# Kernel optimization log

Measured on AMD Instinct MI355X. Metric: run time of the kernel, lower is better.

## Reference

```python
import jax, jax.numpy as jnp
import numpy as np

C = 768      # token feature dim
N = 196      # tokens per stream
R_DIM = 2 * 2 * N  # 784 = concat(A row, A col)


def setup_inputs() -> dict:
    key = jax.random.key(0)
    ks = jax.random.split(key, 16)
    s = 1.0 / np.sqrt(C)
    inp = {
        "x": jax.random.normal(ks[0], (128, N, C), dtype=jnp.float32),
        "y": jax.random.normal(ks[1], (128, N, C), dtype=jnp.float32),
        # linear_conv_1: 1x1 conv (768->768) + BN affine (eval) + ReLU
        "W1": jax.random.normal(ks[2], (C, C), dtype=jnp.float32) * s,
        "b1": jnp.zeros((C,), dtype=jnp.float32),
        "g1": jax.random.uniform(ks[3], (C,), dtype=jnp.float32, minval=0.5, maxval=1.5),
        "be1": jax.random.normal(ks[4], (C,), dtype=jnp.float32) * 0.1,
        # linear_conv_2
        "W2": jax.random.normal(ks[5], (C, C), dtype=jnp.float32) * s,
        "b2": jnp.zeros((C,), dtype=jnp.float32),
        "g2": jax.random.uniform(ks[6], (C,), dtype=jnp.float32, minval=0.5, maxval=1.5),
        "be2": jax.random.normal(ks[7], (C,), dtype=jnp.float32) * 0.1,
        # linear_conv_3: 768->768
        "W3": jax.random.normal(ks[8], (C, C), dtype=jnp.float32) * s,
        "b3": jnp.zeros((C,), dtype=jnp.float32),
        # linear_conv_4: 784->784 over relation rows
        "W4": jax.random.normal(ks[9], (784, 784), dtype=jnp.float32) / np.sqrt(784.0),
        "b4": jnp.zeros((784,), dtype=jnp.float32),
        # linear_conv_5: (768+784)->1
        "W5": jax.random.normal(ks[10], (C + 784, 1), dtype=jnp.float32) / np.sqrt(C + 784.0),
        "b5": jnp.zeros((1,), dtype=jnp.float32),
    }
    return inp


def reference(x, y, W1, b1, g1, be1, W2, b2, g2, be2, W3, b3, W4, b4, W5, b5):
    # per-token 1x1 conv + BN(eval)->affine + ReLU
    phi_x = jax.nn.relu((x @ W1 + b1) * g1 + be1)          # [B,196,768]
    phi_y = jax.nn.relu((y @ W2 + b2) * g2 + be2)          # [B,196,768]
    cat_phi = jnp.concatenate([phi_x, phi_y], axis=1)      # [B,392,768]
    # affinity matrix A = cat_phi @ cat_phi^T
    A = jnp.einsum("bnd,bmd->bnm", cat_phi, cat_phi)       # [B,392,392]
    # R[i] = concat(A[i,:], A[:,i]) -> vectorized as [A | A^T]
    R = jnp.concatenate([A, jnp.swapaxes(A, 1, 2)], axis=2)  # [B,392,784]
    v = cat_phi @ W3 + b3                                   # [B,392,768]
    v_ = R @ W4 + b4                                        # [B,392,784]
    cat_v = jnp.concatenate([v, v_], axis=2)                # [B,392,1552]
    W = cat_v @ W5 + b5                                     # [B,392,1]
    # per-token reweighting then sum of the two streams
    out = x * W[:, :N, :] + y * W[:, N:, :]                 # [B,196,768]
    return out
```

## Files before the change

### kernel.cpp

```cpp
#include <hip/hip_runtime.h>

typedef __bf16 bf16_t;
typedef bf16_t bf16x8 __attribute__((ext_vector_type(8)));
typedef float f32x4 __attribute__((ext_vector_type(4)));
typedef float f32x16 __attribute__((ext_vector_type(16)));
typedef unsigned short u16x8 __attribute__((ext_vector_type(8)));
typedef unsigned short u16x4 __attribute__((ext_vector_type(4)));

#define CD 768
#define NT 196
#define NB 128
#define T2 392
#define MROWS (NB*NT)
#define NTILE 1176

__device__ __forceinline__ unsigned short f2bf(float f){
  unsigned u = __float_as_uint(f);
  u += 0x7fffu + ((u >> 16) & 1u);
  return (unsigned short)(u >> 16);
}
__device__ __forceinline__ float bf2f(unsigned short h){
  return __uint_as_float(((unsigned)h) << 16);
}
__device__ __forceinline__ float wave_reduce(float v){
  #pragma unroll
  for (int o = 32; o > 0; o >>= 1) v += __shfl_down(v, o, 64);
  return v;
}
__device__ __forceinline__ void gload16(const unsigned short* g, unsigned short* l){
  __builtin_amdgcn_global_load_lds(
      (const __attribute__((address_space(1))) unsigned int*)g,
      (__attribute__((address_space(3))) unsigned int*)l, 16, 0, 0);
}

__global__ __launch_bounds__(256) void prep_pack(const float* __restrict__ W1,
                        const float* __restrict__ W2,
                        unsigned short* __restrict__ W1p, unsigned short* __restrict__ W2p){
  __shared__ float tile[64][33];
  const float* src = blockIdx.z ? W2 : W1;
  unsigned short* dst = blockIdx.z ? W2p : W1p;
  const int kt = blockIdx.x, g = blockIdx.y, tid = threadIdx.x;
  #pragma unroll
  for (int e = 0; e < 8; ++e){
    int idx = e*256 + tid;
    int kk = idx >> 5, nn = idx & 31;
    tile[kk][nn] = src[(size_t)(kt*64 + kk)*CD + g*32 + nn];
  }
  __syncthreads();
  const int ks = tid >> 6, lane = tid & 63;
  const int l31 = lane & 31, lh = lane >> 5;
  unsigned short* o = dst + ((size_t)((g*12 + kt)*4 + ks)*64 + lane)*8;
  #pragma unroll
  for (int i = 0; i < 8; ++i)
    o[i] = f2bf(tile[ks*16 + lh*8 + i][l31]);
}

__global__ void prep_u(const float* __restrict__ W3, const float* __restrict__ W4,
                       const float* __restrict__ W5, const float* __restrict__ b3,
                       const float* __restrict__ b4, const float* __restrict__ b5,
                       float* __restrict__ u3, float* __restrict__ u4s, float* __restrict__ cbuf){
  int wid = (blockIdx.x*blockDim.x + threadIdx.x) >> 6;
  int lane = threadIdx.x & 63;
  const float* w5a = W5;
  const float* w5b = W5 + CD;
  float s = 0.f;
  if (wid < CD){
    const float* row = W3 + (size_t)wid*CD;
    for (int k = lane; k < CD; k += 64) s += row[k]*w5a[k];
    s = wave_reduce(s);
    if (lane == 0) u3[wid] = s;
  } else if (wid < CD + T2){
    int j = wid - CD;
    const float* r0 = W4 + (size_t)j*784;
    const float* r1 = W4 + (size_t)(j+T2)*784;
    for (int e = lane; e < 784; e += 64) s += (r0[e]+r1[e])*w5b[e];
    s = wave_reduce(s);
    if (lane == 0) u4s[j] = s;
  } else if (wid == CD + T2){
    for (int k = lane; k < CD; k += 64) s += b3[k]*w5a[k];
    for (int e = lane; e < 784; e += 64) s += b4[e]*w5b[e];
    s = wave_reduce(s);
    if (lane == 0) cbuf[0] = s + b5[0];
  }
}

__global__ void init_t(const float* __restrict__ u3, float* __restrict__ t){
  int i = blockIdx.x*256 + threadIdx.x;
  if (i < (NB+2)*CD) t[i] = (i < NB*CD) ? u3[i % CD] : 0.f;
}

__global__ __launch_bounds__(256) void cvt2(const float* __restrict__ x,
                                            const float* __restrict__ y,
                                            unsigned short* __restrict__ dst){
  const int nv = MROWS*CD/8;
  for (int id = blockIdx.x*256 + threadIdx.x; id < 2*nv; id += gridDim.x*256){
    const float* s = (id < nv) ? x : y;
    int i = (id < nv) ? id : id - nv;
    float4 a = ((const float4*)s)[i*2];
    float4 b = ((const float4*)s)[i*2+1];
    u16x8 o = { f2bf(a.x), f2bf(a.y), f2bf(a.z), f2bf(a.w),
                f2bf(b.x), f2bf(b.y), f2bf(b.z), f2bf(b.w) };
    ((u16x8*)dst)[id] = o;
  }
}

__global__ __launch_bounds__(256, 4) void phi_gemm2(
    const unsigned short* __restrict__ Ax, const unsigned short* __restrict__ Ay,
    const unsigned short* __restrict__ W1p, const unsigned short* __restrict__ W2p,
    const float* __restrict__ biasX, const float* __restrict__ gamX, const float* __restrict__ betX,
    const float* __restrict__ biasY, const float* __restrict__ gamY, const float* __restrict__ betY,
    const float* __restrict__ u4s,
    unsigned short* __restrict__ Px, unsigned short* __restrict__ Py,
    float* __restrict__ t, int mode)
{
  __shared__ unsigned short As[128*64];

  const int tid  = threadIdx.x;
  const int lane = tid & 63;
  const int w    = tid >> 6;
  const int wr = w >> 1, wc = w & 1;

  const int chunk = gridDim.x >> 3;
  int orig = blockIdx.x;
  int swz  = (orig & 7)*chunk + (orig >> 3);
  int s, r;
  if (mode < 0){ s = swz >= NTILE; r = swz - s*NTILE; }
  else         { s = mode; r = swz; }
  const int bn = r % 6;
  const int bm = r / 6;

  const unsigned short* A   = s ? Ay : Ax;
  const unsigned short* Wp  = s ? W2p : W1p;
  const float* bias = s ? biasY : biasX;
  const float* gam  = s ? gamY  : gamX;
  const float* bet  = s ? betY  : betX;
  const float* u4c  = u4s + s*NT;
  unsigned short* phi = s ? Py : Px;

  const int srow = lane >> 3;
  const int p    = lane & 7;
  const int g0   = (p - srow) & 7;
  const unsigned short* a0 = A + (size_t)(bm*128 + w*32 + srow)*CD + g0*8;
  unsigned short* al = &As[(w*32)*64];

  const unsigned short* bb0 = Wp + ((size_t)(bn*4 + wc*2    )*48)*512 + lane*8;
  const unsigned short* bb1 = Wp + ((size_t)(bn*4 + wc*2 + 1)*48)*512 + lane*8;

  const int l31 = lane & 31;
  const int lh  = lane >> 5;
  const int r7  = l31 & 7;

  f32x16 acc[2][2] = {};

  #pragma unroll 1
  for (int kt = 0; kt < 12; ++kt){
    const int ko = kt*64;
    #pragma unroll
    for (int c = 0; c < 4; ++c)
      gload16(a0 + (size_t)c*8*CD + ko, al + c*512);
    bf16x8 bq[2][4];
    #pragma unroll
    for (int ks = 0; ks < 4; ++ks){
      bq[0][ks] = *(const bf16x8*)(bb0 + (kt*4 + ks)*512);
      bq[1][ks] = *(const bf16x8*)(bb1 + (kt*4 + ks)*512);
    }
    __syncthreads();
    #pragma unroll
    for (int ks = 0; ks < 4; ++ks){
      const int phys = ((ks*2 + lh) + r7) & 7;
      bf16x8 af[2];
      #pragma unroll
      for (int mi = 0; mi < 2; ++mi){
        int rr = wr*64 + mi*32 + l31;
        af[mi] = *(const bf16x8*)(&As[rr*64 + phys*8]);
      }
      #pragma unroll
      for (int mi = 0; mi < 2; ++mi)
        #pragma unroll
        for (int nj = 0; nj < 2; ++nj)
          acc[mi][nj] = __builtin_amdgcn_mfma_f32_32x32x16_bf16(af[mi], bq[nj][ks], acc[mi][nj], 0, 0, 0);
    }
    if (kt < 11) __syncthreads();
  }

  const int b_base = (bm*128) / NT;
  int  col0 = bn*128 + wc*64 + l31;
  float bi0 = bias[col0],    ga0 = gam[col0],    be0 = bet[col0];
  float bi1 = bias[col0+32], ga1 = gam[col0+32], be1 = bet[col0+32];
  float cb[2][2] = {{0.f,0.f},{0.f,0.f}};
  #pragma unroll
  for (int mi = 0; mi < 2; ++mi){
    #pragma unroll
    for (int reg = 0; reg < 16; ++reg){
      int rg  = bm*128 + wr*64 + mi*32 + (reg & 3) + 8*(reg >> 2) + 4*lh;
      int b   = rg / NT;
      int tok = rg - b*NT;
      float uw = u4c[tok];
      int bk  = b - b_base;
      #pragma unroll
      for (int nj = 0; nj < 2; ++nj){
        float v = (nj ? (acc[mi][nj][reg] + bi1)*ga1 + be1
                      : (acc[mi][nj][reg] + bi0)*ga0 + be0);
        v = fmaxf(v, 0.f);
        phi[(size_t)rg*CD + col0 + nj*32] = f2bf(v);
        float pv = uw*v;
        cb[nj][0] += (bk == 0) ? pv : 0.f;
        cb[nj][1] += (bk == 1) ? pv : 0.f;
      }
    }
  }
  #pragma unroll
  for (int nj = 0; nj < 2; ++nj){
    cb[nj][0] += __shfl_xor(cb[nj][0], 32, 64);
    cb[nj][1] += __shfl_xor(cb[nj][1], 32, 64);
  }
  if (lane < 32){
    atomicAdd(&t[(size_t)(b_base  )*CD + col0   ], cb[0][0]);
    atomicAdd(&t[(size_t)(b_base+1)*CD + col0   ], cb[0][1]);
    atomicAdd(&t[(size_t)(b_base  )*CD + col0+32], cb[1][0]);
    atomicAdd(&t[(size_t)(b_base+1)*CD + col0+32], cb[1][1]);
  }
}

template<bool USEBF>
__global__ __launch_bounds__(256) void comp_wout(
    const unsigned short* __restrict__ phiX, const unsigned short* __restrict__ phiY,
    const float* __restrict__ t, const float* __restrict__ cbuf,
    const float* __restrict__ x, const float* __restrict__ y,
    const unsigned short* __restrict__ xb, const unsigned short* __restrict__ yb,
    float* __restrict__ out)
{
  int gw   = (blockIdx.x*256 + threadIdx.x) >> 6;
  int lane = threadIdx.x & 63;
  int b = gw / NT;
  const unsigned short* px = phiX + (size_t)gw*CD;
  const unsigned short* py = phiY + (size_t)gw*CD;
  const float* tb = t + (size_t)b*CD;
  float s1 = 0.f, s2 = 0.f;
  #pragma unroll
  for (int it = 0; it < 3; ++it){
    int k = it*256 + lane*4;
    float4 tv = *(const float4*)(tb + k);
    u16x4 ux = *(const u16x4*)(px + k);
    u16x4 uy = *(const u16x4*)(py + k);
    s1 += bf2f(ux.x)*tv.x + bf2f(ux.y)*tv.y + bf2f(ux.z)*tv.z + bf2f(ux.w)*tv.w;
    s2 += bf2f(uy.x)*tv.x + bf2f(uy.y)*tv.y + bf2f(uy.z)*tv.z + bf2f(uy.w)*tv.w;
  }
  s1 = wave_reduce(s1);
  s2 = wave_reduce(s2);
  float cc = cbuf[0];
  float wx = __shfl(s1, 0, 64) + cc;
  float wy = __shfl(s2, 0, 64) + cc;
  float* orow = out + (size_t)gw*CD;
  #pragma unroll
  for (int it = 0; it < 3; ++it){
    int k = it*256 + lane*4;
    float4 xv, yv;
    if (USEBF){
      u16x4 a  = *(const u16x4*)(xb + (size_t)gw*CD + k);
      u16x4 c4 = *(const u16x4*)(yb + (size_t)gw*CD + k);
      xv = float4{bf2f(a.x), bf2f(a.y), bf2f(a.z), bf2f(a.w)};
      yv = float4{bf2f(c4.x), bf2f(c4.y), bf2f(c4.z), bf2f(c4.w)};
    } else {
      xv = *(const float4*)(x + (size_t)gw*CD + k);
      yv = *(const float4*)(y + (size_t)gw*CD + k);
    }
    float4 o;
    o.x = xv.x*wx + yv.x*wy;
    o.y = xv.y*wx + yv.y*wy;
    o.z = xv.z*wx + yv.z*wy;
    o.w = xv.w*wx + yv.w*wy;
    *(float4*)(orow + k) = o;
  }
}

extern "C" void kernel_launch(void* const* d_in, const int* in_sizes, int n_in,
                              void* d_out, int out_size, void* d_ws, size_t ws_size,
                              hipStream_t stream){
  const float* x  = (const float*)d_in[0];
  const float* y  = (const float*)d_in[1];
  const float* W1 = (const float*)d_in[2];
  const float* b1 = (const float*)d_in[3];
  const float* g1 = (const float*)d_in[4];
  const float* be1= (const float*)d_in[5];
  const float* W2 = (const float*)d_in[6];
  const float* b2 = (const float*)d_in[7];
  const float* g2 = (const float*)d_in[8];
  const float* be2= (const float*)d_in[9];
  const float* W3 = (const float*)d_in[10];
  const float* b3 = (const float*)d_in[11];
  const float* W4 = (const float*)d_in[12];
  const float* b4 = (const float*)d_in[13];
  const float* W5 = (const float*)d_in[14];
  const float* b5 = (const float*)d_in[15];
  float* out = (float*)d_out;

  const size_t BIGE = (size_t)MROWS*CD;
  const size_t smallF = CD + T2 + 4 + (size_t)(NB+2)*CD;
  const size_t need4 = (2*(size_t)CD*CD + 4*BIGE)*2 + smallF*4 + 256;
  const bool big = (ws_size >= need4);

  unsigned short* W1p = (unsigned short*)d_ws;
  unsigned short* W2p = W1p + CD*CD;
  unsigned short* Sx  = W2p + CD*CD;
  unsigned short* Sy  = Sx + BIGE;
  unsigned short* Px, * Py;
  float* smalls;
  if (big){
    Px = Sy + BIGE;
    Py = Px + BIGE;
    smalls = (float*)(Py + BIGE);
  } else {
    Px = Sy + BIGE;
    Py = Sx;
    smalls = (float*)(Px + BIGE);
  }
  float* u3   = smalls;
  float* u4s  = u3 + CD;
  float* cbuf = u4s + T2;
  float* t    = cbuf + 4;

  prep_pack<<<dim3(12,24,2), 256, 0, stream>>>(W1, W2, W1p, W2p);
  prep_u<<<(CD + T2 + 4)/4, 256, 0, stream>>>(W3, W4, W5, b3, b4, b5, u3, u4s, cbuf);
  init_t<<<((NB+2)*CD + 255)/256, 256, 0, stream>>>(u3, t);

  cvt2<<<2048, 256, 0, stream>>>(x, y, Sx);

  if (big){
    phi_gemm2<<<2*NTILE, 256, 0, stream>>>(Sx, Sy, W1p, W2p,
        b1, g1, be1, b2, g2, be2, u4s, Px, Py, t, -1);
    comp_wout<true><<<MROWS/4, 256, 0, stream>>>(Px, Py, t, cbuf, x, y, Sx, Sy, out);
  } else {
    phi_gemm2<<<NTILE, 256, 0, stream>>>(Sx, Sy, W1p, W2p,
        b1, g1, be1, b2, g2, be2, u4s, Px, Py, t, 0);
    phi_gemm2<<<NTILE, 256, 0, stream>>>(Sx, Sy, W1p, W2p,
        b1, g1, be1, b2, g2, be2, u4s, Px, Py, t, 1);
    comp_wout<false><<<MROWS/4, 256, 0, stream>>>(Px, Py, t, cbuf, x, y, Sx, Sy, out);
  }
}
```

Before: 181.5 us.

## Fuse fp32-to-bf16 conversion into phi GEMM A-tile loads

Removes the separate cvt2 pass that wrote bf16 copies of x and y. The GEMM now streams fp32 x/y directly into LDS with a 16-slot XOR-style swizzle and converts to bf16 when building MFMA fragments. B-fragment loads move inside the ks loop. The final kernel reads fp32 x/y instead of bf16 copies, and the small-workspace fallback path is dropped. The LDS A tile doubles to 32KB, which may lower occupancy, and each K step issues twice as many global-to-LDS loads.

```diff
diff --git a/kernel.cpp b/kernel.cpp
--- a/kernel.cpp
+++ b/kernel.cpp
@@ -27,7 +27,7 @@
   for (int o = 32; o > 0; o >>= 1) v += __shfl_down(v, o, 64);
   return v;
 }
-__device__ __forceinline__ void gload16(const unsigned short* g, unsigned short* l){
+__device__ __forceinline__ void gload16(const void* g, void* l){
   __builtin_amdgcn_global_load_lds(
       (const __attribute__((address_space(1))) unsigned int*)g,
       (__attribute__((address_space(3))) unsigned int*)l, 16, 0, 0);
@@ -89,31 +89,16 @@
   if (i < (NB+2)*CD) t[i] = (i < NB*CD) ? u3[i % CD] : 0.f;
 }
 
-__global__ __launch_bounds__(256) void cvt2(const float* __restrict__ x,
-                                            const float* __restrict__ y,
-                                            unsigned short* __restrict__ dst){
-  const int nv = MROWS*CD/8;
-  for (int id = blockIdx.x*256 + threadIdx.x; id < 2*nv; id += gridDim.x*256){
-    const float* s = (id < nv) ? x : y;
-    int i = (id < nv) ? id : id - nv;
-    float4 a = ((const float4*)s)[i*2];
-    float4 b = ((const float4*)s)[i*2+1];
-    u16x8 o = { f2bf(a.x), f2bf(a.y), f2bf(a.z), f2bf(a.w),
-                f2bf(b.x), f2bf(b.y), f2bf(b.z), f2bf(b.w) };
-    ((u16x8*)dst)[id] = o;
-  }
-}
-
 __global__ __launch_bounds__(256, 4) void phi_gemm2(
-    const unsigned short* __restrict__ Ax, const unsigned short* __restrict__ Ay,
+    const float* __restrict__ X, const float* __restrict__ Y,
     const unsigned short* __restrict__ W1p, const unsigned short* __restrict__ W2p,
     const float* __restrict__ biasX, const float* __restrict__ gamX, const float* __restrict__ betX,
     const float* __restrict__ biasY, const float* __restrict__ gamY, const float* __restrict__ betY,
     const float* __restrict__ u4s,
     unsigned short* __restrict__ Px, unsigned short* __restrict__ Py,
-    float* __restrict__ t, int mode)
+    float* __restrict__ t)
 {
-  __shared__ unsigned short As[128*64];
+  __shared__ float As[128*64];
 
   const int tid  = threadIdx.x;
   const int lane = tid & 63;
@@ -123,32 +108,27 @@
   const int chunk = gridDim.x >> 3;
   int orig = blockIdx.x;
   int swz  = (orig & 7)*chunk + (orig >> 3);
-  int s, r;
-  if (mode < 0){ s = swz >= NTILE; r = swz - s*NTILE; }
-  else         { s = mode; r = swz; }
+  const int s = swz >= NTILE;
+  const int r = swz - s*NTILE;
   const int bn = r % 6;
   const int bm = r / 6;
 
-  const unsigned short* A   = s ? Ay : Ax;
-  const unsigned short* Wp  = s ? W2p : W1p;
+  const float* A  = s ? Y : X;
+  const unsigned short* Wp = s ? W2p : W1p;
   const float* bias = s ? biasY : biasX;
   const float* gam  = s ? gamY  : gamX;
   const float* bet  = s ? betY  : betX;
   const float* u4c  = u4s + s*NT;
   unsigned short* phi = s ? Py : Px;
 
-  const int srow = lane >> 3;
-  const int p    = lane & 7;
-  const int g0   = (p - srow) & 7;
-  const unsigned short* a0 = A + (size_t)(bm*128 + w*32 + srow)*CD + g0*8;
-  unsigned short* al = &As[(w*32)*64];
+  const int srow4 = lane >> 4;
+  const int p16   = lane & 15;
 
   const unsigned short* bb0 = Wp + ((size_t)(bn*4 + wc*2    )*48)*512 + lane*8;
   const unsigned short* bb1 = Wp + ((size_t)(bn*4 + wc*2 + 1)*48)*512 + lane*8;
 
   const int l31 = lane & 31;
   const int lh  = lane >> 5;
-  const int r7  = l31 & 7;
 
   f32x16 acc[2][2] = {};
 
@@ -156,29 +136,34 @@
   for (int kt = 0; kt < 12; ++kt){
     const int ko = kt*64;
     #pragma unroll
-    for (int c = 0; c < 4; ++c)
-      gload16(a0 + (size_t)c*8*CD + ko, al + c*512);
-    bf16x8 bq[2][4];
-    #pragma unroll
-    for (int ks = 0; ks < 4; ++ks){
-      bq[0][ks] = *(const bf16x8*)(bb0 + (kt*4 + ks)*512);
-      bq[1][ks] = *(const bf16x8*)(bb1 + (kt*4 + ks)*512);
+    for (int c = 0; c < 8; ++c){
+      int row_l = w*32 + c*4 + srow4;
+      int g = (p16 - row_l) & 15;
+      gload16(A + (size_t)(bm*128 + row_l)*CD + ko + g*4,
+              &As[(w*32 + c*4)*64]);
     }
     __syncthreads();
     #pragma unroll
     for (int ks = 0; ks < 4; ++ks){
-      const int phys = ((ks*2 + lh) + r7) & 7;
+      bf16x8 bq0 = *(const bf16x8*)(bb0 + (kt*4 + ks)*512);
+      bf16x8 bq1 = *(const bf16x8*)(bb1 + (kt*4 + ks)*512);
       bf16x8 af[2];
       #pragma unroll
       for (int mi = 0; mi < 2; ++mi){
-        int rr = wr*64 + mi*32 + l31;
-        af[mi] = *(const bf16x8*)(&As[rr*64 + phys*8]);
+        int row = wr*64 + mi*32 + l31;
+        int s0 = ks*4 + lh*2;
+        const float* rp = &As[row*64];
+        f32x4 lo = *(const f32x4*)(rp + ((s0     + row) & 15)*4);
+        f32x4 hi = *(const f32x4*)(rp + ((s0 + 1 + row) & 15)*4);
+        bf16x8 a_;
+        #pragma unroll
+        for (int i = 0; i < 4; ++i){ a_[i] = (bf16_t)lo[i]; a_[4+i] = (bf16_t)hi[i]; }
+        af[mi] = a_;
       }
-      #pragma unroll
-      for (int mi = 0; mi < 2; ++mi)
-        #pragma unroll
-        for (int nj = 0; nj < 2; ++nj)
-          acc[mi][nj] = __builtin_amdgcn_mfma_f32_32x32x16_bf16(af[mi], bq[nj][ks], acc[mi][nj], 0, 0, 0);
+      acc[0][0] = __builtin_amdgcn_mfma_f32_32x32x16_bf16(af[0], bq0, acc[0][0], 0, 0, 0);
+      acc[0][1] = __builtin_amdgcn_mfma_f32_32x32x16_bf16(af[0], bq1, acc[0][1], 0, 0, 0);
+      acc[1][0] = __builtin_amdgcn_mfma_f32_32x32x16_bf16(af[1], bq0, acc[1][0], 0, 0, 0);
+      acc[1][1] = __builtin_amdgcn_mfma_f32_32x32x16_bf16(af[1], bq1, acc[1][1], 0, 0, 0);
     }
     if (kt < 11) __syncthreads();
   }
@@ -222,12 +207,10 @@
   }
 }
 
-template<bool USEBF>
 __global__ __launch_bounds__(256) void comp_wout(
     const unsigned short* __restrict__ phiX, const unsigned short* __restrict__ phiY,
     const float* __restrict__ t, const float* __restrict__ cbuf,
     const float* __restrict__ x, const float* __restrict__ y,
-    const unsigned short* __restrict__ xb, const unsigned short* __restrict__ yb,
     float* __restrict__ out)
 {
   int gw   = (blockIdx.x*256 + threadIdx.x) >> 6;
@@ -251,20 +234,14 @@
   float cc = cbuf[0];
   float wx = __shfl(s1, 0, 64) + cc;
   float wy = __shfl(s2, 0, 64) + cc;
+  const float* xr = x + (size_t)gw*CD;
+  const float* yr = y + (size_t)gw*CD;
   float* orow = out + (size_t)gw*CD;
   #pragma unroll
   for (int it = 0; it < 3; ++it){
     int k = it*256 + lane*4;
-    float4 xv, yv;
-    if (USEBF){
-      u16x4 a  = *(const u16x4*)(xb + (size_t)gw*CD + k);
-      u16x4 c4 = *(const u16x4*)(yb + (size_t)gw*CD + k);
-      xv = float4{bf2f(a.x), bf2f(a.y), bf2f(a.z), bf2f(a.w)};
-      yv = float4{bf2f(c4.x), bf2f(c4.y), bf2f(c4.z), bf2f(c4.w)};
-    } else {
-      xv = *(const float4*)(x + (size_t)gw*CD + k);
-      yv = *(const float4*)(y + (size_t)gw*CD + k);
-    }
+    float4 xv = *(const float4*)(xr + k);
+    float4 yv = *(const float4*)(yr + k);
     float4 o;
     o.x = xv.x*wx + yv.x*wy;
     o.y = xv.y*wx + yv.y*wy;
@@ -296,26 +273,12 @@
   float* out = (float*)d_out;
 
   const size_t BIGE = (size_t)MROWS*CD;
-  const size_t smallF = CD + T2 + 4 + (size_t)(NB+2)*CD;
-  const size_t need4 = (2*(size_t)CD*CD + 4*BIGE)*2 + smallF*4 + 256;
-  const bool big = (ws_size >= need4);
 
   unsigned short* W1p = (unsigned short*)d_ws;
   unsigned short* W2p = W1p + CD*CD;
-  unsigned short* Sx  = W2p + CD*CD;
-  unsigned short* Sy  = Sx + BIGE;
-  unsigned short* Px, * Py;
-  float* smalls;
-  if (big){
-    Px = Sy + BIGE;
-    Py = Px + BIGE;
-    smalls = (float*)(Py + BIGE);
-  } else {
-    Px = Sy + BIGE;
-    Py = Sx;
-    smalls = (float*)(Px + BIGE);
-  }
-  float* u3   = smalls;
+  unsigned short* Px  = W2p + CD*CD;
+  unsigned short* Py  = Px + BIGE;
+  float* u3   = (float*)(Py + BIGE);
   float* u4s  = u3 + CD;
   float* cbuf = u4s + T2;
   float* t    = cbuf + 4;
@@ -324,17 +287,8 @@
   prep_u<<<(CD + T2 + 4)/4, 256, 0, stream>>>(W3, W4, W5, b3, b4, b5, u3, u4s, cbuf);
   init_t<<<((NB+2)*CD + 255)/256, 256, 0, stream>>>(u3, t);
 
-  cvt2<<<2048, 256, 0, stream>>>(x, y, Sx);
-
-  if (big){
-    phi_gemm2<<<2*NTILE, 256, 0, stream>>>(Sx, Sy, W1p, W2p,
-        b1, g1, be1, b2, g2, be2, u4s, Px, Py, t, -1);
-    comp_wout<true><<<MROWS/4, 256, 0, stream>>>(Px, Py, t, cbuf, x, y, Sx, Sy, out);
-  } else {
-    phi_gemm2<<<NTILE, 256, 0, stream>>>(Sx, Sy, W1p, W2p,
-        b1, g1, be1, b2, g2, be2, u4s, Px, Py, t, 0);
-    phi_gemm2<<<NTILE, 256, 0, stream>>>(Sx, Sy, W1p, W2p,
-        b1, g1, be1, b2, g2, be2, u4s, Px, Py, t, 1);
-    comp_wout<false><<<MROWS/4, 256, 0, stream>>>(Px, Py, t, cbuf, x, y, Sx, Sy, out);
-  }
-}
+  phi_gemm2<<<2*NTILE, 256, 0, stream>>>(x, y, W1p, W2p,
+      b1, g1, be1, b2, g2, be2, u4s, Px, Py, t);
+
+  comp_wout<<<MROWS/4, 256, 0, stream>>>(Px, Py, t, cbuf, x, y, out);
+}
```

Result: no change. 184.1 us (+1.4%).

## Double phi GEMM K-tile to 128 and prefetch weight fragments one step ahead

Applied to the files above, without the earlier changes.

The phi GEMM now stages 128-wide K slices of the activation tile in LDS instead of 64-wide ones. The XOR-style swizzle is widened from 8 to 16 chunks so the rotation stays consistent between the global-to-LDS writes and the fragment reads. This halves the number of K iterations and barriers. Weight fragments are no longer loaded four at a time before the barrier; they are fetched one k-step ahead of their use in registers. The cost is twice the LDS per block (32KB), which may reduce occupancy, and each barrier period has a longer load phase.

```diff
diff --git a/kernel.cpp b/kernel.cpp
--- a/kernel.cpp
+++ b/kernel.cpp
@@ -27,7 +27,7 @@
   for (int o = 32; o > 0; o >>= 1) v += __shfl_down(v, o, 64);
   return v;
 }
-__device__ __forceinline__ void gload16(const unsigned short* g, unsigned short* l){
+__device__ __forceinline__ void gload16(const void* g, void* l){
   __builtin_amdgcn_global_load_lds(
       (const __attribute__((address_space(1))) unsigned int*)g,
       (__attribute__((address_space(3))) unsigned int*)l, 16, 0, 0);
@@ -113,7 +113,7 @@
     unsigned short* __restrict__ Px, unsigned short* __restrict__ Py,
     float* __restrict__ t, int mode)
 {
-  __shared__ unsigned short As[128*64];
+  __shared__ unsigned short As[128*128];
 
   const int tid  = threadIdx.x;
   const int lane = tid & 63;
@@ -129,58 +129,61 @@
   const int bn = r % 6;
   const int bm = r / 6;
 
-  const unsigned short* A   = s ? Ay : Ax;
-  const unsigned short* Wp  = s ? W2p : W1p;
+  const unsigned short* A  = s ? Ay : Ax;
+  const unsigned short* Wp = s ? W2p : W1p;
   const float* bias = s ? biasY : biasX;
   const float* gam  = s ? gamY  : gamX;
   const float* bet  = s ? betY  : betX;
   const float* u4c  = u4s + s*NT;
   unsigned short* phi = s ? Py : Px;
 
-  const int srow = lane >> 3;
-  const int p    = lane & 7;
-  const int g0   = (p - srow) & 7;
-  const unsigned short* a0 = A + (size_t)(bm*128 + w*32 + srow)*CD + g0*8;
-  unsigned short* al = &As[(w*32)*64];
+  const int srow2 = lane >> 4;
+  const int p16   = lane & 15;
+  const int rowb  = w*32 + srow2;
+  const int g0    = (p16 - rowb) & 15;
+  const unsigned short* aB = A + (size_t)(bm*128 + rowb)*CD;
+  unsigned short* alB = &As[rowb & 0x60 ? 0 : 0];
+  (void)alB;
 
   const unsigned short* bb0 = Wp + ((size_t)(bn*4 + wc*2    )*48)*512 + lane*8;
   const unsigned short* bb1 = Wp + ((size_t)(bn*4 + wc*2 + 1)*48)*512 + lane*8;
 
   const int l31 = lane & 31;
   const int lh  = lane >> 5;
-  const int r7  = l31 & 7;
 
   f32x16 acc[2][2] = {};
 
   #pragma unroll 1
-  for (int kt = 0; kt < 12; ++kt){
-    const int ko = kt*64;
+  for (int kt = 0; kt < 6; ++kt){
+    const int ko = kt*128;
     #pragma unroll
-    for (int c = 0; c < 4; ++c)
-      gload16(a0 + (size_t)c*8*CD + ko, al + c*512);
-    bf16x8 bq[2][4];
-    #pragma unroll
-    for (int ks = 0; ks < 4; ++ks){
-      bq[0][ks] = *(const bf16x8*)(bb0 + (kt*4 + ks)*512);
-      bq[1][ks] = *(const bf16x8*)(bb1 + (kt*4 + ks)*512);
+    for (int c = 0; c < 8; ++c){
+      gload16(aB + (size_t)c*4*CD + ko + (((g0 - 4*c) & 15)*8),
+              &As[(w*32 + c*4)*128]);
     }
+    bf16x8 bqa0 = *(const bf16x8*)(bb0 + (kt*8    )*512);
+    bf16x8 bqa1 = *(const bf16x8*)(bb1 + (kt*8    )*512);
     __syncthreads();
     #pragma unroll
-    for (int ks = 0; ks < 4; ++ks){
-      const int phys = ((ks*2 + lh) + r7) & 7;
+    for (int ks = 0; ks < 8; ++ks){
+      bf16x8 bqb0, bqb1;
+      if (ks < 7){
+        bqb0 = *(const bf16x8*)(bb0 + (kt*8 + ks + 1)*512);
+        bqb1 = *(const bf16x8*)(bb1 + (kt*8 + ks + 1)*512);
+      }
       bf16x8 af[2];
       #pragma unroll
       for (int mi = 0; mi < 2; ++mi){
-        int rr = wr*64 + mi*32 + l31;
-        af[mi] = *(const bf16x8*)(&As[rr*64 + phys*8]);
+        int row = wr*64 + mi*32 + l31;
+        af[mi] = *(const bf16x8*)(&As[row*128 + (((ks*2 + lh) + row) & 15)*8]);
       }
-      #pragma unroll
-      for (int mi = 0; mi < 2; ++mi)
-        #pragma unroll
-        for (int nj = 0; nj < 2; ++nj)
-          acc[mi][nj] = __builtin_amdgcn_mfma_f32_32x32x16_bf16(af[mi], bq[nj][ks], acc[mi][nj], 0, 0, 0);
+      acc[0][0] = __builtin_amdgcn_mfma_f32_32x32x16_bf16(af[0], bqa0, acc[0][0], 0, 0, 0);
+      acc[0][1] = __builtin_amdgcn_mfma_f32_32x32x16_bf16(af[0], bqa1, acc[0][1], 0, 0, 0);
+      acc[1][0] = __builtin_amdgcn_mfma_f32_32x32x16_bf16(af[1], bqa0, acc[1][0], 0, 0, 0);
+      acc[1][1] = __builtin_amdgcn_mfma_f32_32x32x16_bf16(af[1], bqa1, acc[1][1], 0, 0, 0);
+      bqa0 = bqb0; bqa1 = bqb1;
     }
-    if (kt < 11) __syncthreads();
+    if (kt < 5) __syncthreads();
   }
 
   const int b_base = (bm*128) / NT;
```

Result: no change. 181.4 us (-0.0%).
